# Optimization experiments

Hardware: AMD Instinct MI355X
Metric: run time of the kernel (lower is better)

## Reference

```python
import jax, jax.numpy as jnp
import numpy as np


def _rotate_matrices(angles):
    # angles: (M, 1) -> rot (M, 2, 2), rows [[c, -s], [s, c]]
    c = jnp.cos(angles)
    s = jnp.sin(angles)
    rot = jnp.stack([jnp.concatenate([c, -s], axis=1),
                     jnp.concatenate([s, c], axis=1)], axis=1)
    return rot, jnp.swapaxes(rot, 1, 2)


def _seq_group_permute(x, mapping, perms, final=False):
    # x: (B, S, d), perms: (d//2, 2, 2)
    B, S, d = x.shape
    if not final:
        x = x[:, :, mapping]
    x = x.reshape(B, S, d // 2, 2)
    x = jnp.einsum('ijmk,mkn->ijmn', x, perms).reshape(B, S, d)
    if final:
        x = x[:, :, mapping]
    return x


def _mat_group_permute_inv(m, mapping, perms_inv, transposed):
    # m: (R, d), perms_inv: (d//2, 2, 2)
    R, d = m.shape
    m = m[:, mapping].reshape(R, d // 2, 2)
    sub = 'imk,mkn->imn' if transposed else 'imk,mnk->imn'
    return jnp.einsum(sub, m, perms_inv).reshape(R, d)


def setup_inputs() -> dict:
    key = jax.random.key(0)
    ks = jax.random.split(key, 8)
    B, S, IN, OUT = 4, 2048, 1024, 4096
    inp = jax.random.normal(ks[0], (B, S, IN), dtype=jnp.float32)
    weight = jax.random.normal(ks[1], (OUT, IN), dtype=jnp.float32) * 0.02
    mask = (jax.random.uniform(ks[2], (OUT, IN)) > 0.5).astype(jnp.float32)
    in_scores = jax.random.normal(ks[3], (IN // 2, 1), dtype=jnp.float32)
    out_scores = jax.random.normal(ks[4], (OUT // 2, 1), dtype=jnp.float32)
    in_mapping = jax.random.permutation(ks[5], IN).astype(jnp.int32)
    out_mapping = jax.random.permutation(ks[6], OUT).astype(jnp.int32)
    out_mapping_reverse = jnp.argsort(out_mapping).astype(jnp.int32)
    return {
        'input': inp,
        'weight': weight,
        'mask': mask,
        'in_permutation_scores': in_scores,
        'out_permutation_scores': out_scores,
        'in_mapping': in_mapping,
        'out_mapping': out_mapping,
        'out_mapping_reverse': out_mapping_reverse,
        'temperature': 1,
    }


def reference(input, weight, mask, in_permutation_scores, out_permutation_scores,
              in_mapping, out_mapping, out_mapping_reverse, temperature):
    in_permut, in_permut_inv = _rotate_matrices(in_permutation_scores)
    out_permut, out_permut_inv = _rotate_matrices(out_permutation_scores)
    # permute + rotate activations on the input side
    s_in = _seq_group_permute(input, in_mapping, in_permut)
    # inverse permute/rotate the weight's input dim, then its output dim
    m2 = _mat_group_permute_inv(weight, in_mapping, in_permut_inv, transposed=False)
    m3 = _mat_group_permute_inv(m2.T, out_mapping, out_permut_inv, transposed=True)
    m3 = m3 * mask.T  # (in, out)
    s_inner = jnp.einsum('bsi,io->bso', s_in, m3)
    s_out = _seq_group_permute(s_inner, out_mapping_reverse, out_permut, final=True)
    return s_out
```

## Files before the change

### kernel.cpp

```cpp
#include <hip/hip_runtime.h>
#include <hip/hip_bf16.h>
#include <stdint.h>

#define M_DIM 8192
#define K_DIM 1024
#define N_DIM 4096

typedef __bf16 bf16x8 __attribute__((ext_vector_type(8)));
typedef float  f32x4  __attribute__((ext_vector_type(4)));

__device__ __forceinline__ uint16_t f2bf(float f) {
  union { float f; uint32_t u; } x; x.f = f;
  uint32_t u = x.u;
  return (uint16_t)((u + 0x7FFFu + ((u >> 16) & 1u)) >> 16);
}

__global__ __launch_bounds__(256) void convert_bf16_kernel(
    const float* __restrict__ in, uint16_t* __restrict__ out, int n4) {
  int i = blockIdx.x * 256 + threadIdx.x;
  if (i >= n4) return;
  float4 v = ((const float4*)in)[i];
  ushort4 o;
  o.x = f2bf(v.x); o.y = f2bf(v.y); o.z = f2bf(v.z); o.w = f2bf(v.w);
  ((ushort4*)out)[i] = o;
}

__global__ __launch_bounds__(256) void build_w_kernel(
    const float* __restrict__ weight,
    const float* __restrict__ mask,
    const float* __restrict__ in_scores,
    const float* __restrict__ out_scores,
    const int*   __restrict__ in_mapping,
    const int*   __restrict__ out_mapping,
    uint16_t*    __restrict__ w5t)
{
  __shared__ float    w0[K_DIM], w1[K_DIM];
  __shared__ uint16_t o0[K_DIM], o1[K_DIM];

  const int mo = blockIdx.x;
  const int t  = threadIdx.x;

  const int r0 = out_mapping[2 * mo];
  const int r1 = out_mapping[2 * mo + 1];

  ((float4*)w0)[t] = ((const float4*)(weight + (size_t)r0 * K_DIM))[t];
  ((float4*)w1)[t] = ((const float4*)(weight + (size_t)r1 * K_DIM))[t];

  const float ao = out_scores[mo];
  const float so = sinf(ao), co = cosf(ao);

  __syncthreads();

#pragma unroll
  for (int s = 0; s < 2; s++) {
    const int mi = t + s * 256;
    const float ai = in_scores[mi];
    const float si = sinf(ai), ci = cosf(ai);
    const int ia0 = in_mapping[2 * mi];
    const int ia1 = in_mapping[2 * mi + 1];

    const float w00 = w0[ia0], w01 = w0[ia1];
    const float w10 = w1[ia0], w11 = w1[ia1];

    float a00 =  ci * w00 + si * w01;
    float a01 = -si * w00 + ci * w01;
    float a10 =  ci * w10 + si * w11;
    float a11 = -si * w10 + ci * w11;

    float b00 = co * a00 - so * a10;
    float b10 = co * a01 - so * a11;
    float b01 = so * a00 + co * a10;
    float b11 = so * a01 + co * a11;

    const float2 mk0 = *(const float2*)&mask[(size_t)(2 * mo) * K_DIM + 2 * mi];
    const float2 mk1 = *(const float2*)&mask[(size_t)(2 * mo + 1) * K_DIM + 2 * mi];
    b00 *= mk0.x; b10 *= mk0.y;
    b01 *= mk1.x; b11 *= mk1.y;

    float c00 =  co * b00 + so * b01;
    float c10 =  co * b10 + so * b11;
    float c01 = -so * b00 + co * b01;
    float c11 = -so * b10 + co * b11;

    o0[ia0] = f2bf(ci * c00 - si * c10);
    o0[ia1] = f2bf(si * c00 + ci * c10);
    o1[ia0] = f2bf(ci * c01 - si * c11);
    o1[ia1] = f2bf(si * c01 + ci * c11);
  }

  __syncthreads();

  ((uint2*)(w5t + (size_t)r0 * K_DIM))[t] = ((const uint2*)o0)[t];
  ((uint2*)(w5t + (size_t)r1 * K_DIM))[t] = ((const uint2*)o1)[t];
}


__device__ __forceinline__ void async_load16(const uint16_t* g, uint16_t* lds_wave_uniform) {
  __builtin_amdgcn_global_load_lds(
      (const __attribute__((address_space(1))) uint32_t*)g,
      (__attribute__((address_space(3))) uint32_t*)lds_wave_uniform,
      16, 0, 0);
}

__global__ __launch_bounds__(512, 2) void gemm_kernel(
    const uint16_t* __restrict__ A,
    const uint16_t* __restrict__ BT,
    float* __restrict__ C)
{
  __shared__ __align__(16) uint16_t As[2][2][128 * 64];
  __shared__ __align__(16) uint16_t Bs[2][2][128 * 64];

  const int tid  = threadIdx.x;
  const int w    = tid >> 6;
  const int lane = tid & 63;
  const int quad = lane >> 4;
  const int rr   = lane & 15;
  const int wm   = w >> 2;
  const int wn   = w & 3;
  const int hA   = wm;
  const int hB   = wn >> 1;

  const int flat = blockIdx.y * gridDim.x + blockIdx.x;
  const int swz  = ((flat & 7) << 6) | (flat >> 3);
  const int bm   = swz >> 4;
  const int bn   = swz & 15;

  f32x4 acc[8][4] = {};

  const uint16_t* gA[2];
  const uint16_t* gB[2];
#pragma unroll
  for (int ii = 0; ii < 2; ii++) {
    const int c   = ii * 512 + tid;
    const int row = c >> 3;
    const int g   = (c & 7) ^ (row & 7);
    gA[ii] = A  + (size_t)(bm * 256 + row) * K_DIM + g * 8;
    gB[ii] = BT + (size_t)(bn * 256 + row) * K_DIM + g * 8;
  }

#define STAGE_A(BUF, H, KT)                                                   \
  do {                                                                        \
    _Pragma("unroll")                                                         \
    for (int ii_ = 0; ii_ < 2; ii_++)                                         \
      async_load16(gA[ii_] + (H) * (128 * K_DIM) + (KT) * 64,                 \
                   &As[BUF][H][(ii_ * 512 + w * 64) * 8]);                    \
  } while (0)

#define STAGE_B(BUF, H, KT)                                                   \
  do {                                                                        \
    _Pragma("unroll")                                                         \
    for (int ii_ = 0; ii_ < 2; ii_++)                                         \
      async_load16(gB[ii_] + (H) * (128 * K_DIM) + (KT) * 64,                 \
                   &Bs[BUF][H][(ii_ * 512 + w * 64) * 8]);                    \
  } while (0)

  int offA[8][2], offB[4][2];
#pragma unroll
  for (int i = 0; i < 8; i++) {
    const int r = i * 16 + rr;
#pragma unroll
    for (int s = 0; s < 2; s++) {
      const int gk = s * 4 + quad;
      offA[i][s] = (r * 8 + (gk ^ (r & 7))) * 8;
    }
  }
#pragma unroll
  for (int j = 0; j < 4; j++) {
    const int r = (wn & 1) * 64 + j * 16 + rr;
#pragma unroll
    for (int s = 0; s < 2; s++) {
      const int gk = s * 4 + quad;
      offB[j][s] = (r * 8 + (gk ^ (r & 7))) * 8;
    }
  }

#define PHASE(P, EXTRA_READS, STAGE_STMT, PRE_BARRIER_WAITS)                   \
  {                                                                            \
    bf16x8 af[2][2];                                                           \
    EXTRA_READS;                                                               \
    _Pragma("unroll")                                                          \
    for (int d_ = 0; d_ < 2; d_++)                                             \
      _Pragma("unroll")                                                        \
      for (int s_ = 0; s_ < 2; s_++)                                           \
        af[d_][s_] = *reinterpret_cast<const bf16x8*>(asb + offA[2*(P)+d_][s_]); \
    STAGE_STMT;                                                                \
    PRE_BARRIER_WAITS;                                                         \
    __builtin_amdgcn_s_barrier();                                              \
    asm volatile("s_waitcnt lgkmcnt(0)" ::: "memory");                         \
    __builtin_amdgcn_sched_barrier(0);                                         \
    __builtin_amdgcn_s_setprio(1);                                             \
    _Pragma("unroll")                                                          \
    for (int s_ = 0; s_ < 2; s_++)                                             \
      _Pragma("unroll")                                                        \
      for (int d_ = 0; d_ < 2; d_++)                                           \
        _Pragma("unroll")                                                      \
        for (int j_ = 0; j_ < 4; j_++)                                         \
          acc[2*(P)+d_][j_] = __builtin_amdgcn_mfma_f32_16x16x32_bf16(         \
              af[d_][s_], bfv[j_][s_], acc[2*(P)+d_][j_], 0, 0, 0);            \
    __builtin_amdgcn_s_setprio(0);                                             \
    __builtin_amdgcn_s_barrier();                                              \
  }

  STAGE_B(0, 0, 0); STAGE_B(0, 1, 0);
  STAGE_A(0, 0, 0); STAGE_A(0, 1, 0);
  STAGE_B(1, 0, 1); STAGE_B(1, 1, 1);
  asm volatile("s_waitcnt vmcnt(4)" ::: "memory");
  __builtin_amdgcn_s_barrier();

  for (int t = 0; t < 16; ++t) {
    const int buf  = t & 1;
    const int nbuf = buf ^ 1;
    const uint16_t* asb = &As[buf][hA][0];
    const uint16_t* bsb = &Bs[buf][hB][0];

    bf16x8 bfv[4][2];

    PHASE(0,
          { _Pragma("unroll")
            for (int j_ = 0; j_ < 4; j_++)
              _Pragma("unroll")
              for (int s_ = 0; s_ < 2; s_++)
                bfv[j_][s_] = *reinterpret_cast<const bf16x8*>(bsb + offB[j_][s_]); },
          { if (t < 15) STAGE_A(nbuf, 0, t + 1); },
          { asm volatile("s_waitcnt lgkmcnt(8)" ::: "memory"); });
    PHASE(1, {}, { if (t < 15) STAGE_A(nbuf, 1, t + 1); }, {});
    PHASE(2, {}, { if (t < 14) STAGE_B(buf, 0, t + 2); }, {});
    PHASE(3, {}, { if (t < 14) STAGE_B(buf, 1, t + 2); },
          { if (t < 14)       { asm volatile("s_waitcnt vmcnt(4)" ::: "memory"); }
            else if (t == 14) { asm volatile("s_waitcnt vmcnt(0)" ::: "memory"); } });
  }

#undef PHASE
#undef STAGE_A
#undef STAGE_B

#pragma unroll
  for (int i = 0; i < 8; i++) {
    const int row0 = bm * 256 + wm * 128 + i * 16 + quad * 4;
#pragma unroll
    for (int j = 0; j < 4; j++) {
      const int col = bn * 256 + wn * 64 + j * 16 + rr;
#pragma unroll
      for (int rg = 0; rg < 4; rg++) {
        C[(size_t)(row0 + rg) * N_DIM + col] = acc[i][j][rg];
      }
    }
  }
}

extern "C" void kernel_launch(void* const* d_in, const int* in_sizes, int n_in,
                              void* d_out, int out_size, void* d_ws, size_t ws_size,
                              hipStream_t stream) {
  const float* input      = (const float*)d_in[0];
  const float* weight     = (const float*)d_in[1];
  const float* mask       = (const float*)d_in[2];
  const float* in_scores  = (const float*)d_in[3];
  const float* out_scores = (const float*)d_in[4];
  const int*   in_mapping = (const int*)d_in[5];
  const int*   out_mapping= (const int*)d_in[6];
  float* out = (float*)d_out;

  uint16_t* a_bf16 = (uint16_t*)d_ws;
  uint16_t* w5t    = (uint16_t*)d_ws + (size_t)M_DIM * K_DIM;

  convert_bf16_kernel<<<(M_DIM * K_DIM / 4 + 255) / 256, 256, 0, stream>>>(
      input, a_bf16, M_DIM * K_DIM / 4);

  build_w_kernel<<<2048, 256, 0, stream>>>(
      weight, mask, in_scores, out_scores, in_mapping, out_mapping, w5t);

  dim3 grid(N_DIM / 256, M_DIM / 256);
  gemm_kernel<<<grid, 512, 0, stream>>>(a_bf16, w5t, out);
}
```

Before: 262.6 us.

## Software-pipeline LDS fragment reads one phase ahead with double-buffered registers

Restructures the GEMM main loop so that the LDS reads of A and B fragments for the next phase (and the next tile) are issued after the barrier, alongside the current phase's MFMAs. They land in ping-pong register buffers (afA/afB, bfvA/bfvB). The loop is unrolled by two tiles, and the tail tiles get special modes that adjust the vmcnt waits. This aims to hide LDS latency behind MFMA work, at the cost of higher VGPR pressure and more complicated wait bookkeeping.

Result: faster. 254.4 us (-3.1%).

```diff
diff --git a/kernel.cpp b/kernel.cpp
--- a/kernel.cpp
+++ b/kernel.cpp
@@ -174,31 +174,61 @@
     }
   }
 
-#define PHASE(P, EXTRA_READS, STAGE_STMT, PRE_BARRIER_WAITS)                   \
-  {                                                                            \
-    bf16x8 af[2][2];                                                           \
-    EXTRA_READS;                                                               \
-    _Pragma("unroll")                                                          \
-    for (int d_ = 0; d_ < 2; d_++)                                             \
-      _Pragma("unroll")                                                        \
-      for (int s_ = 0; s_ < 2; s_++)                                           \
-        af[d_][s_] = *reinterpret_cast<const bf16x8*>(asb + offA[2*(P)+d_][s_]); \
-    STAGE_STMT;                                                                \
-    PRE_BARRIER_WAITS;                                                         \
-    __builtin_amdgcn_s_barrier();                                              \
-    asm volatile("s_waitcnt lgkmcnt(0)" ::: "memory");                         \
-    __builtin_amdgcn_sched_barrier(0);                                         \
-    __builtin_amdgcn_s_setprio(1);                                             \
-    _Pragma("unroll")                                                          \
-    for (int s_ = 0; s_ < 2; s_++)                                             \
-      _Pragma("unroll")                                                        \
-      for (int d_ = 0; d_ < 2; d_++)                                           \
-        _Pragma("unroll")                                                      \
-        for (int j_ = 0; j_ < 4; j_++)                                         \
-          acc[2*(P)+d_][j_] = __builtin_amdgcn_mfma_f32_16x16x32_bf16(         \
-              af[d_][s_], bfv[j_][s_], acc[2*(P)+d_][j_], 0, 0, 0);            \
-    __builtin_amdgcn_s_setprio(0);                                             \
-    __builtin_amdgcn_s_barrier();                                              \
+#define PF_A(AF, ASB, R)                                                      \
+  _Pragma("unroll")                                                           \
+  for (int d_ = 0; d_ < 2; d_++)                                              \
+    _Pragma("unroll")                                                         \
+    for (int s_ = 0; s_ < 2; s_++)                                            \
+      AF[d_][s_] = *reinterpret_cast<const bf16x8*>((ASB) + offA[(R) + d_][s_]);
+
+#define PF_B(BN, BSB)                                                         \
+  _Pragma("unroll")                                                           \
+  for (int j_ = 0; j_ < 4; j_++)                                              \
+    _Pragma("unroll")                                                         \
+    for (int s_ = 0; s_ < 2; s_++)                                            \
+      BN[j_][s_] = *reinterpret_cast<const bf16x8*>((BSB) + offB[j_][s_]);
+
+#define MFMA16(AF, R, BV)                                                     \
+  _Pragma("unroll")                                                           \
+  for (int s_ = 0; s_ < 2; s_++)                                              \
+    _Pragma("unroll")                                                         \
+    for (int d_ = 0; d_ < 2; d_++)                                            \
+      _Pragma("unroll")                                                       \
+      for (int j_ = 0; j_ < 4; j_++)                                          \
+        acc[(R) + d_][j_] = __builtin_amdgcn_mfma_f32_16x16x32_bf16(          \
+            AF[d_][s_], BV[j_][s_], acc[(R) + d_][j_], 0, 0, 0);
+
+#define PHASE(STAGE_STMT, WAIT_STMT, PF_STMT, AF, RBASE, BV)                  \
+  {                                                                           \
+    STAGE_STMT;                                                               \
+    WAIT_STMT;                                                                \
+    __builtin_amdgcn_s_barrier();                                             \
+    asm volatile("s_waitcnt lgkmcnt(0)" ::: "memory");                        \
+    __builtin_amdgcn_sched_barrier(0);                                        \
+    __builtin_amdgcn_s_setprio(1);                                            \
+    PF_STMT;                                                                  \
+    MFMA16(AF, RBASE, BV);                                                    \
+    __builtin_amdgcn_s_setprio(0);                                            \
+    __builtin_amdgcn_s_barrier();                                             \
+  }
+
+#define TILE(T, BV, BN, MODE)                                                 \
+  {                                                                           \
+    const int buf_ = (T) & 1;                                                 \
+    const uint16_t* asb_  = &As[buf_][hA][0];                                 \
+    const uint16_t* asb_n = &As[buf_ ^ 1][hA][0];                             \
+    const uint16_t* bsb_n = &Bs[buf_ ^ 1][hB][0];                             \
+    PHASE({ if (MODE < 2) STAGE_A(buf_ ^ 1, 0, (T) + 1); }, {},               \
+          { PF_A(afB, asb_, 2) }, afA, 0, BV);                                \
+    PHASE({ if (MODE < 2) STAGE_A(buf_ ^ 1, 1, (T) + 1); }, {},               \
+          { PF_A(afA, asb_, 4) }, afB, 2, BV);                                \
+    PHASE({ if (MODE == 0) STAGE_B(buf_, 0, (T) + 2); },                      \
+          { if (MODE == 0)      { asm volatile("s_waitcnt vmcnt(2)" ::: "memory"); } \
+            else if (MODE == 1) { asm volatile("s_waitcnt vmcnt(0)" ::: "memory"); } }, \
+          { PF_A(afB, asb_, 6) }, afA, 4, BV);                                \
+    PHASE({ if (MODE == 0) STAGE_B(buf_, 1, (T) + 2); }, {},                  \
+          { if (MODE < 2) { PF_A(afA, asb_n, 0) PF_B(BN, bsb_n) } },          \
+          afB, 6, BV);                                                        \
   }
 
   STAGE_B(0, 0, 0); STAGE_B(0, 1, 0);
@@ -207,30 +237,22 @@
   asm volatile("s_waitcnt vmcnt(4)" ::: "memory");
   __builtin_amdgcn_s_barrier();
 
-  for (int t = 0; t < 16; ++t) {
-    const int buf  = t & 1;
-    const int nbuf = buf ^ 1;
-    const uint16_t* asb = &As[buf][hA][0];
-    const uint16_t* bsb = &Bs[buf][hB][0];
-
-    bf16x8 bfv[4][2];
-
-    PHASE(0,
-          { _Pragma("unroll")
-            for (int j_ = 0; j_ < 4; j_++)
-              _Pragma("unroll")
-              for (int s_ = 0; s_ < 2; s_++)
-                bfv[j_][s_] = *reinterpret_cast<const bf16x8*>(bsb + offB[j_][s_]); },
-          { if (t < 15) STAGE_A(nbuf, 0, t + 1); },
-          { asm volatile("s_waitcnt lgkmcnt(8)" ::: "memory"); });
-    PHASE(1, {}, { if (t < 15) STAGE_A(nbuf, 1, t + 1); }, {});
-    PHASE(2, {}, { if (t < 14) STAGE_B(buf, 0, t + 2); }, {});
-    PHASE(3, {}, { if (t < 14) STAGE_B(buf, 1, t + 2); },
-          { if (t < 14)       { asm volatile("s_waitcnt vmcnt(4)" ::: "memory"); }
-            else if (t == 14) { asm volatile("s_waitcnt vmcnt(0)" ::: "memory"); } });
-  }
-
+  bf16x8 afA[2][2], afB[2][2], bfvA[4][2], bfvB[4][2];
+  PF_A(afA, (&As[0][hA][0]), 0);
+  PF_B(bfvA, (&Bs[0][hB][0]));
+
+  for (int t = 0; t < 14; t += 2) {
+    TILE(t,     bfvA, bfvB, 0);
+    TILE(t + 1, bfvB, bfvA, 0);
+  }
+  TILE(14, bfvA, bfvB, 1);
+  TILE(15, bfvB, bfvB, 2);
+
+#undef TILE
 #undef PHASE
+#undef MFMA16
+#undef PF_A
+#undef PF_B
 #undef STAGE_A
 #undef STAGE_B
 
```
